# Performance work log

Hardware: AMD Instinct MI355X
Metric: run time of the kernel (lower is better)

Reference implementation:

```python
import jax, jax.numpy as jnp
import numpy as np

B, T, V, L = 32, 1000, 1024, 128
BLANK = 0
NEG = -1e30  # log-space -inf surrogate (fp32 safe)


def setup_inputs() -> dict:
    key = jax.random.key(0)
    k1, k2 = jax.random.split(key)
    hs_pad = jax.random.normal(k1, (B, T, V), dtype=jnp.float32)
    h_lens = jnp.full((B,), T, dtype=jnp.int32)
    ys_pad = jax.random.randint(k2, (B, L), 1, V, dtype=jnp.int32)  # blank=0 excluded
    ys_lens = jnp.full((B,), L, dtype=jnp.int32)
    return {"hs_pad": hs_pad, "h_lens": h_lens, "ys_pad": ys_pad, "ys_lens": ys_lens}


def ctc_loss(hs_pad, h_lens, ys_pad, ys_lens):
    """log_softmax + CTC forward (alpha) DP, 'mean' reduction like torch.nn.CTCLoss."""
    logp = jax.nn.log_softmax(hs_pad, axis=-1)          # (B, T, V)
    Bsz, Tm, _ = hs_pad.shape
    Lm = ys_pad.shape[1]
    S = 2 * Lm + 1                                       # extended label lattice width
    # Extended label sequence: blank, y1, blank, y2, ..., yL, blank
    ext = jnp.zeros((Bsz, S), ys_pad.dtype).at[:, 1::2].set(ys_pad)
    # Gather log-probs at extended labels: (B, T, S)
    lp_ext = jnp.take_along_axis(logp, jnp.broadcast_to(ext[:, None, :], (Bsz, Tm, S)), axis=2)
    # Skip transition s-2 -> s allowed iff ext[s] != blank and ext[s] != ext[s-2]
    ext_m2 = jnp.pad(ext, ((0, 0), (2, 0)), constant_values=BLANK)[:, :S]
    skip = (ext != BLANK) & (ext != ext_m2) & (jnp.arange(S)[None, :] >= 2)

    # alpha at t=0: only lattice positions 0 (blank) and 1 (first label)
    alpha0 = (jnp.full((Bsz, S), NEG, dtype=logp.dtype)
              .at[:, 0].set(lp_ext[:, 0, 0])
              .at[:, 1].set(lp_ext[:, 0, 1]))

    def step(alpha, xs):
        lp_t, t = xs                                     # lp_t: (B, S)
        a1 = alpha
        a2 = jnp.pad(alpha, ((0, 0), (1, 0)), constant_values=NEG)[:, :S]
        a3 = jnp.where(skip, jnp.pad(alpha, ((0, 0), (2, 0)), constant_values=NEG)[:, :S], NEG)
        new = jnp.logaddexp(jnp.logaddexp(a1, a2), a3) + lp_t
        active = (t < h_lens)[:, None]                   # freeze alpha past each h_len
        return jnp.where(active, new, alpha), None

    lp_seq = jnp.moveaxis(lp_ext, 1, 0)[1:]              # (T-1, B, S)
    ts = jnp.arange(1, Tm)
    alpha, _ = jax.lax.scan(step, alpha0, (lp_seq, ts))

    # Final log-likelihood: last blank (2*len) or last label (2*len - 1)
    idx_blank = (2 * ys_lens)[:, None]
    idx_label = (2 * ys_lens - 1)[:, None]
    a_end = jnp.logaddexp(jnp.take_along_axis(alpha, idx_blank, axis=1)[:, 0],
                          jnp.take_along_axis(alpha, idx_label, axis=1)[:, 0])
    loss = -a_end                                        # (B,)
    # torch 'mean': per-sample loss divided by target length, then batch mean
    return jnp.mean(loss / ys_lens.astype(loss.dtype))


def reference(hs_pad, h_lens, ys_pad, ys_lens):
    return ctc_loss(hs_pad, h_lens, ys_pad, ys_lens)
```

## Files before the change

kernel.cpp:

```cpp
#include <hip/hip_runtime.h>
#include <math.h>

constexpr int Bc = 32;
constexpr int Tc = 1000;
constexpr int Vc = 1024;
constexpr int Lc = 128;
constexpr int Sc = 2 * Lc + 1;
constexpr int SP = 320;
constexpr float NEGF = -1e30f;
constexpr float L2E = 1.4426950408889634f;
constexpr float LN2 = 0.6931471805599453f;
constexpr int ENEG = -(1 << 24);

#if __has_builtin(__builtin_amdgcn_exp2f)
#define EXP2F(x) __builtin_amdgcn_exp2f(x)
#else
#define EXP2F(x) exp2f(x)
#endif
#if __has_builtin(__builtin_amdgcn_logf)
#define LOG2F(x) __builtin_amdgcn_logf(x)
#else
#define LOG2F(x) log2f(x)
#endif
#if __has_builtin(__builtin_amdgcn_ldexpf)
#define LDEXPF(x, e) __builtin_amdgcn_ldexpf(x, e)
#else
#define LDEXPF(x, e) ldexpf(x, e)
#endif
#if __has_builtin(__builtin_amdgcn_frexp_expf)
#define FREXPE(x) __builtin_amdgcn_frexp_expf(x)
#else
__device__ inline int FREXPE(float x) { int e; (void)frexpf(x, &e); return e; }
#endif

__device__ __forceinline__ float dpp_wave_shr1(float x) {
  return __int_as_float(__builtin_amdgcn_update_dpp(
      0, __float_as_int(x), 0x138 , 0xf, 0xf, true));
}
__device__ __forceinline__ int dpp_wave_shr1_i(int x) {
  return __builtin_amdgcn_update_dpp(0, x, 0x138 , 0xf, 0xf, true);
}


__global__ __launch_bounds__(256) void ctc_lse_gather(
    const float* __restrict__ hs, const int* __restrict__ ys,
    float* __restrict__ lpe) {
  const int wv = threadIdx.x >> 6;
  const int lane = threadIdx.x & 63;
  const int bt = blockIdx.x * 4 + wv;
  const int b = bt / Tc;
  const float* row = hs + (size_t)bt * Vc;

  __shared__ float xs_all[4][Vc];
  float* xs = xs_all[wv];

  float4 v[4];
#pragma unroll
  for (int q = 0; q < 4; ++q) v[q] = reinterpret_cast<const float4*>(row)[lane + 64 * q];
#pragma unroll
  for (int q = 0; q < 4; ++q) { v[q].x *= L2E; v[q].y *= L2E; v[q].z *= L2E; v[q].w *= L2E; }

  float m = -3.4e38f;
#pragma unroll
  for (int q = 0; q < 4; ++q)
    m = fmaxf(m, fmaxf(fmaxf(v[q].x, v[q].y), fmaxf(v[q].z, v[q].w)));
#pragma unroll
  for (int off = 32; off; off >>= 1) m = fmaxf(m, __shfl_xor(m, off, 64));

  float sum = 0.f;
#pragma unroll
  for (int q = 0; q < 4; ++q)
    sum += EXP2F(v[q].x - m) + EXP2F(v[q].y - m) + EXP2F(v[q].z - m) + EXP2F(v[q].w - m);
#pragma unroll
  for (int off = 32; off; off >>= 1) sum += __shfl_xor(sum, off, 64);
  const float lse2 = m + LOG2F(sum);

#pragma unroll
  for (int q = 0; q < 4; ++q) reinterpret_cast<float4*>(xs)[lane + 64 * q] = v[q];
  __syncthreads();

  float* out = lpe + (size_t)bt * SP;
#pragma unroll
  for (int j = 0; j < 4; ++j) {
    const int s = 4 * lane + j;
    const int lab = (s & 1) ? ys[b * Lc + (s >> 1)] : 0;
    out[j * 64 + lane] = EXP2F(xs[lab] - lse2);
  }
  out[256 + lane] = (lane == 63) ? EXP2F(xs[0] - lse2) : 0.f;
}

__global__ __launch_bounds__(64) void ctc_alpha(
    const float* __restrict__ lpe, const int* __restrict__ ys,
    const int* __restrict__ hlen, const int* __restrict__ ylen,
    float* __restrict__ lossb) {
  const int b = blockIdx.x;
  const int lane = threadIdx.x;
  const float* pb = lpe + (size_t)b * Tc * SP;
  const int* yb = ys + b * Lc;

  const float sk1 = (lane >= 1 && yb[2 * lane - 1] != yb[2 * lane]) ? 1.f : 0.f;
  const float sk3 = (yb[2 * lane] != yb[2 * lane + 1]) ? 1.f : 0.f;

  float m0 = (lane == 0) ? pb[0] : 0.f;
  float m1 = (lane == 0) ? pb[64] : 0.f;
  float m2 = 0.f, m3 = 0.f, m4 = 0.f;
  int E = (lane == 0) ? 0 : ENEG;
  float fsh = 0.f;

  const int Te = min(hlen[b], Tc);

  auto renorm = [&]() {
    const float mx = fmaxf(fmaxf(fmaxf(m0, m1), fmaxf(m2, m3)), m4);
    const int e = FREXPE(mx);
    const int E1 = (mx > 0.f) ? E + e : ENEG;
    int Eup = dpp_wave_shr1_i(E1);
    if (lane == 0) Eup = ENEG;
    const int En = max(E1, Eup);
    const int dm = E - En;
    fsh = LDEXPF(1.f, Eup - En);
    m0 = LDEXPF(m0, dm);
    m1 = LDEXPF(m1, dm);
    m2 = LDEXPF(m2, dm);
    m3 = LDEXPF(m3, dm);
    m4 = LDEXPF(m4, dm);
    E = En;
  };

  auto step = [&](const float* p) {
    const float msh = dpp_wave_shr1(m3);
    const float am = msh * fsh;
    const float n0 = (m0 + am) * p[0];
    const float n1 = fmaf(sk1, am, m1 + m0) * p[1];
    const float n2 = (m2 + m1) * p[2];
    const float n3 = fmaf(sk3, m1, m3 + m2) * p[3];
    const float n4 = (m4 + m3) * p[4];
    m0 = n0; m1 = n1; m2 = n2; m3 = n3; m4 = n4;
  };

  float bufA[8][5], bufB[8][5];
  auto load8A = [&](int trow) {
    const float* p = pb + (size_t)trow * SP + lane;
#pragma unroll
    for (int k = 0; k < 8; ++k)
#pragma unroll
      for (int j = 0; j < 5; ++j) bufA[k][j] = p[k * SP + j * 64];
  };
  auto load8B = [&](int trow) {
    const float* p = pb + (size_t)trow * SP + lane;
#pragma unroll
    for (int k = 0; k < 8; ++k)
#pragma unroll
      for (int j = 0; j < 5; ++j) bufB[k][j] = p[k * SP + j * 64];
  };

  int t = 1;
  if (t + 8 <= Te) load8A(t);
  while (t + 16 <= Te) {
    load8B(t + 8);
    renorm();
#pragma unroll
    for (int k = 0; k < 8; ++k) step(bufA[k]);
    t += 8;
    if (t + 16 <= Te) load8A(t + 8);
    renorm();
#pragma unroll
    for (int k = 0; k < 8; ++k) step(bufB[k]);
    t += 8;
  }
  if (t + 8 <= Te) {
    renorm();
#pragma unroll
    for (int k = 0; k < 8; ++k) step(bufA[k]);
    t += 8;
  }
  while (t < Te) {
    float lp[5];
#pragma unroll
    for (int j = 0; j < 5; ++j) lp[j] = pb[(size_t)t * SP + j * 64 + lane];
    renorm();
    step(lp);
    ++t;
  }

  __shared__ float msm[SP];
  __shared__ int esm[64];
#pragma unroll
  for (int j = 0; j < 4; ++j) msm[4 * lane + j] = (j == 0 ? m0 : j == 1 ? m1 : j == 2 ? m2 : m3);
  if (lane == 63) msm[256] = m4;
  esm[lane] = E;
  __syncthreads();
  if (lane == 0) {
    const int yl = ylen[b];
    const int s1 = 2 * yl, s0 = 2 * yl - 1;
    const int l1 = (s1 == 256) ? 63 : (s1 >> 2);
    const int l0 = s0 >> 2;
    const float vx = msm[s1]; const int ex = esm[l1];
    const float vy = msm[s0]; const int ey = esm[l0];
    const int Em = max(ex, ey);
    const float r = LDEXPF(vx, ex - Em) + LDEXPF(vy, ey - Em);
    const float ae2 = (r > 0.f) ? (LOG2F(r) + (float)Em) : NEGF;
    lossb[b] = -(ae2 * LN2) / (float)yl;
  }
}

__global__ __launch_bounds__(64) void ctc_final(
    const float* __restrict__ lossb, float* __restrict__ out) {
  const int lane = threadIdx.x;
  float v = (lane < Bc) ? lossb[lane] : 0.f;
#pragma unroll
  for (int off = 32; off; off >>= 1) v += __shfl_xor(v, off, 64);
  if (lane == 0) out[0] = v * (1.f / (float)Bc);
}

extern "C" void kernel_launch(void* const* d_in, const int* in_sizes, int n_in,
                              void* d_out, int out_size, void* d_ws, size_t ws_size,
                              hipStream_t stream) {
  const float* hs = (const float*)d_in[0];
  const int* hlen = (const int*)d_in[1];
  const int* ys = (const int*)d_in[2];
  const int* ylen = (const int*)d_in[3];
  float* out = (float*)d_out;

  float* lpe = (float*)d_ws;
  float* lossb = lpe + (size_t)Bc * Tc * SP;

  ctc_lse_gather<<<Bc * Tc / 4, 256, 0, stream>>>(hs, ys, lpe);
  ctc_alpha<<<Bc, 64, 0, stream>>>(lpe, ys, hlen, ylen, lossb);
  ctc_final<<<1, 64, 0, stream>>>(lossb, out);
}
```

Measured before the change: 248.3 us.

## Interleave lattice probs per lane and triple-buffer alpha row prefetch

The gather kernel now writes each lane's five extended-label probabilities contiguously at a 512-float row stride, instead of in five 64-wide planes. The alpha kernel can then fetch each timestep with one float4 plus one scalar load rather than five scattered loads. The alpha loop also moves from two to three 8-step register buffers, so loads are issued two groups ahead, and it gets a rewritten tail. The aim is to hide global memory latency in the serial DP recurrence, at the cost of more registers and a larger, sparser workspace whose writes only partly fill cache lines.

```diff
diff --git a/kernel.cpp b/kernel.cpp
--- a/kernel.cpp
+++ b/kernel.cpp
@@ -6,7 +6,7 @@
 constexpr int Vc = 1024;
 constexpr int Lc = 128;
 constexpr int Sc = 2 * Lc + 1;
-constexpr int SP = 320;
+constexpr int SPn = 512;
 constexpr float NEGF = -1e30f;
 constexpr float L2E = 1.4426950408889634f;
 constexpr float LN2 = 0.6931471805599453f;
@@ -79,14 +79,18 @@
   for (int q = 0; q < 4; ++q) reinterpret_cast<float4*>(xs)[lane + 64 * q] = v[q];
   __syncthreads();
 
-  float* out = lpe + (size_t)bt * SP;
-#pragma unroll
-  for (int j = 0; j < 4; ++j) {
-    const int s = 4 * lane + j;
-    const int lab = (s & 1) ? ys[b * Lc + (s >> 1)] : 0;
-    out[j * 64 + lane] = EXP2F(xs[lab] - lse2);
-  }
-  out[256 + lane] = (lane == 63) ? EXP2F(xs[0] - lse2) : 0.f;
+  float* out = lpe + (size_t)bt * SPn + lane * 8;
+  float4 o;
+  {
+    const int la1 = ys[b * Lc + 2 * lane];
+    const int la3 = ys[b * Lc + 2 * lane + 1];
+    o.x = EXP2F(xs[0] - lse2);
+    o.y = EXP2F(xs[la1] - lse2);
+    o.z = EXP2F(xs[0] - lse2);
+    o.w = EXP2F(xs[la3] - lse2);
+  }
+  *reinterpret_cast<float4*>(out) = o;
+  out[4] = (lane == 63) ? o.x : 0.f;
 }
 
 __global__ __launch_bounds__(64) void ctc_alpha(
@@ -95,14 +99,15 @@
     float* __restrict__ lossb) {
   const int b = blockIdx.x;
   const int lane = threadIdx.x;
-  const float* pb = lpe + (size_t)b * Tc * SP;
+  const float* pb = lpe + (size_t)b * Tc * SPn;
+  const float* pl = pb + lane * 8;
   const int* yb = ys + b * Lc;
 
   const float sk1 = (lane >= 1 && yb[2 * lane - 1] != yb[2 * lane]) ? 1.f : 0.f;
   const float sk3 = (yb[2 * lane] != yb[2 * lane + 1]) ? 1.f : 0.f;
 
   float m0 = (lane == 0) ? pb[0] : 0.f;
-  float m1 = (lane == 0) ? pb[64] : 0.f;
+  float m1 = (lane == 0) ? pb[1] : 0.f;
   float m2 = 0.f, m3 = 0.f, m4 = 0.f;
   int E = (lane == 0) ? 0 : ENEG;
   float fsh = 0.f;
@@ -137,52 +142,57 @@
     m0 = n0; m1 = n1; m2 = n2; m3 = n3; m4 = n4;
   };
 
-  float bufA[8][5], bufB[8][5];
-  auto load8A = [&](int trow) {
-    const float* p = pb + (size_t)trow * SP + lane;
-#pragma unroll
-    for (int k = 0; k < 8; ++k)
-#pragma unroll
-      for (int j = 0; j < 5; ++j) bufA[k][j] = p[k * SP + j * 64];
-  };
-  auto load8B = [&](int trow) {
-    const float* p = pb + (size_t)trow * SP + lane;
-#pragma unroll
-    for (int k = 0; k < 8; ++k)
-#pragma unroll
-      for (int j = 0; j < 5; ++j) bufB[k][j] = p[k * SP + j * 64];
-  };
-
-  int t = 1;
-  if (t + 8 <= Te) load8A(t);
-  while (t + 16 <= Te) {
-    load8B(t + 8);
-    renorm();
-#pragma unroll
-    for (int k = 0; k < 8; ++k) step(bufA[k]);
-    t += 8;
-    if (t + 16 <= Te) load8A(t + 8);
-    renorm();
-#pragma unroll
-    for (int k = 0; k < 8; ++k) step(bufB[k]);
-    t += 8;
-  }
-  if (t + 8 <= Te) {
-    renorm();
-#pragma unroll
-    for (int k = 0; k < 8; ++k) step(bufA[k]);
-    t += 8;
-  }
-  while (t < Te) {
-    float lp[5];
-#pragma unroll
-    for (int j = 0; j < 5; ++j) lp[j] = pb[(size_t)t * SP + j * 64 + lane];
-    renorm();
-    step(lp);
-    ++t;
-  }
-
-  __shared__ float msm[SP];
+  float bufA[8][5], bufB[8][5], bufC[8][5];
+#define LOAD8(BUF, TROW)                                                      \
+  do {                                                                        \
+    const float* p_ = pl + (size_t)(TROW)*SPn;                                \
+    _Pragma("unroll") for (int k_ = 0; k_ < 8; ++k_) {                        \
+      const float4 v_ = *reinterpret_cast<const float4*>(p_ + k_ * SPn);      \
+      BUF[k_][0] = v_.x; BUF[k_][1] = v_.y;                                   \
+      BUF[k_][2] = v_.z; BUF[k_][3] = v_.w;                                   \
+      BUF[k_][4] = p_[k_ * SPn + 4];                                          \
+    }                                                                         \
+  } while (0)
+#define STEP8(BUF)                                                            \
+  do {                                                                        \
+    renorm();                                                                 \
+    _Pragma("unroll") for (int k_ = 0; k_ < 8; ++k_) step(BUF[k_]);           \
+  } while (0)
+
+  const int G = (Te - 1) / 8;
+  int t = 1, g = 0;
+  if (G > 0) LOAD8(bufA, 1);
+  if (G > 1) LOAD8(bufB, 9);
+  while (g + 3 <= G) {
+    LOAD8(bufC, t + 16);
+    STEP8(bufA); t += 8;
+    if (g + 3 < G) LOAD8(bufA, t + 16);
+    STEP8(bufB); t += 8;
+    if (g + 4 < G) LOAD8(bufB, t + 16);
+    STEP8(bufC); t += 8;
+    g += 3;
+  }
+  if (G - g >= 1) { STEP8(bufA); t += 8; }
+  if (G - g >= 2) { STEP8(bufB); t += 8; }
+  {
+    const int R = Te - t;
+#pragma unroll
+    for (int k = 0; k < 7; ++k)
+      if (k < R) {
+        const float* p_ = pl + (size_t)(t + k) * SPn;
+        const float4 v_ = *reinterpret_cast<const float4*>(p_);
+        bufC[k][0] = v_.x; bufC[k][1] = v_.y;
+        bufC[k][2] = v_.z; bufC[k][3] = v_.w;
+        bufC[k][4] = p_[4];
+      }
+#pragma unroll
+    for (int k = 0; k < 7; ++k)
+      if (k < R) { renorm(); step(bufC[k]); }
+  }
+#undef LOAD8
+#undef STEP8
+
+  __shared__ float msm[Sc];
   __shared__ int esm[64];
 #pragma unroll
   for (int j = 0; j < 4; ++j) msm[4 * lane + j] = (j == 0 ? m0 : j == 1 ? m1 : j == 2 ? m2 : m3);
@@ -222,7 +232,7 @@
   float* out = (float*)d_out;
 
   float* lpe = (float*)d_ws;
-  float* lossb = lpe + (size_t)Bc * Tc * SP;
+  float* lossb = lpe + (size_t)Bc * Tc * SPn;
 
   ctc_lse_gather<<<Bc * Tc / 4, 256, 0, stream>>>(hs, ys, lpe);
   ctc_alpha<<<Bc, 64, 0, stream>>>(lpe, ys, hlen, ylen, lossb);
```

After: 283.3 us. 14.1% more time.
